# Optimization experiments

Hardware: AMD Instinct MI355X
Metric: run time of the kernel (lower is better)

Reference implementation:

```python
import jax, jax.numpy as jnp
import numpy as np

# Model / shape constants (match init_kwargs and input_specs)
E, H, N, B = 1024, 16, 4096, 4
D = E // H               # head_dim = 64
W_SZ, EXT, C_SZ = 128, 128, 128   # window, ext window, rf chunk
NEG = -1e9


def _linear(x, w, b):
    # torch nn.Linear convention: w is (out, in)
    return x @ w.T + b


def _layernorm(x, g, b, eps=1e-5):
    m = jnp.mean(x, -1, keepdims=True)
    v = jnp.mean((x - m) ** 2, -1, keepdims=True)
    return (x - m) * jax.lax.rsqrt(v + eps) * g + b


def _ext_windows(x, w, ext):
    # x: (b,h,n,d) -> (b,h,g,ext+w,d); window g covers keys [g*w-ext, g*w+w)
    # (front-padded with zeros, same as causal_window_1d_partition + as_strided)
    g = x.shape[2] // w
    xp = jnp.pad(x, ((0, 0), (0, 0), (ext, 0), (0, 0)))
    idx = jnp.arange(g)[:, None] * w + jnp.arange(ext + w)[None, :]
    return xp[:, :, idx]


def setup_inputs() -> dict:
    key = jax.random.key(0)
    ks = jax.random.split(key, 20)
    p = lambda i, shape: jax.random.normal(ks[i], shape, jnp.float32) * 0.02
    return {
        'query': jax.random.normal(ks[0], (N, B, E), jnp.float32),
        'Wq': p(1, (E, E)), 'bq': jnp.zeros((E,), jnp.float32),
        'Wk': p(2, (E, E)), 'bk': jnp.zeros((E,), jnp.float32),
        'Wv': p(3, (E, E)), 'bv': jnp.zeros((E,), jnp.float32),
        'Wo': p(4, (E, E)), 'bo': jnp.zeros((E,), jnp.float32),
        'mu_q_w': p(5, (D, D)), 'mu_q_b': jnp.zeros((D,), jnp.float32),
        'mu_q_g': jnp.ones((D,), jnp.float32), 'mu_q_be': jnp.zeros((D,), jnp.float32),
        'mu_k_w': p(6, (D, D)), 'mu_k_b': jnp.zeros((D,), jnp.float32),
        'mu_k_g': jnp.ones((D,), jnp.float32), 'mu_k_be': jnp.zeros((D,), jnp.float32),
    }


def reference(query, Wq, bq, Wk, bk, Wv, bv, Wo, bo,
              mu_q_w, mu_q_b, mu_q_g, mu_q_be,
              mu_k_w, mu_k_b, mu_k_g, mu_k_be):
    n, b, e = query.shape
    h, d = H, D
    scaling = d ** -0.5

    q = _linear(query, Wq, bq)
    k = _linear(query, Wk, bk)
    v = _linear(query, Wv, bv)
    to_bhnd = lambda t: jnp.transpose(t.reshape(n, b, h, d), (1, 2, 0, 3))
    q, k, v = to_bhnd(q), to_bhnd(k), to_bhnd(v)
    q = q * scaling

    # ---------------- local causal windowed attention scores ----------------
    g = n // W_SZ
    w_q = q.reshape(b, h, g, W_SZ, d)
    w_k = _ext_windows(k, W_SZ, EXT)   # (b,h,g,EXT+W,d)
    w_v = _ext_windows(v, W_SZ, EXT)
    local_dots = jnp.einsum('bhgid,bhgjd->bhgij', w_q, w_k)
    i = jnp.arange(W_SZ)[:, None]
    j = jnp.arange(EXT + W_SZ)[None, :]
    causal_ok = j <= i + EXT                      # key pos <= query pos
    gi = jnp.arange(g)[:, None, None]
    valid = j[None] >= (EXT - gi * W_SZ)          # mask zero-padded front keys
    local_mask = causal_ok[None] & valid          # (g, W, EXT+W)
    local_dots = jnp.where(local_mask[None, None], local_dots, NEG)

    # ------------- random-feature (EVA) chunk-level global branch -------------
    nc = n // C_SZ
    rf_q = q.reshape(b, h, nc, C_SZ, d)
    rf_k = k.reshape(b, h, nc, C_SZ, d)
    rf_v = v.reshape(b, h, nc, C_SZ, d)
    rf_q_bar = _layernorm(_linear(rf_q.mean(-2), mu_q_w, mu_q_b), mu_q_g, mu_q_be)
    rf_k_bar = _layernorm(_linear(rf_k.mean(-2), mu_k_w, mu_k_b), mu_k_g, mu_k_be)
    mu = rf_q_bar + rf_k_bar   # eval mode: weights = mu (no Gaussian noise)

    # prm_projection(rf_k, mu) with normalize=False, then softmax within chunk
    norm = scaling * jnp.sum(rf_k ** 2, -1) / 2.0            # (b,h,nc,p)
    log_proj_k = jnp.einsum('bhcd,bhcpd->bhcp', mu, rf_k) * scaling - norm
    beta = jax.nn.softmax(log_proj_k, -1)
    rfa_chunk = jnp.einsum('bhcp,bhcpd->bhcd', beta, rf_v)   # SNIS chunk values

    rfa_dots = jnp.einsum('bhgid,bhcd->bhgic', w_q, rf_k_bar)
    # chunk c visible to window g iff the whole chunk precedes the window
    chunk_vis = (jnp.arange(nc)[None, :] + 1) * C_SZ <= jnp.arange(g)[:, None] * W_SZ
    rfa_dots = jnp.where(chunk_vis[None, None, :, None, :], rfa_dots, NEG)

    # joint softmax over [local keys | global chunk pseudo-keys]
    attn = jax.nn.softmax(jnp.concatenate([local_dots, rfa_dots], -1), -1)
    la, ga = attn[..., : EXT + W_SZ], attn[..., EXT + W_SZ:]
    out = jnp.einsum('bhgij,bhgjd->bhgid', la, w_v) \
        + jnp.einsum('bhgic,bhcd->bhgid', ga, rfa_chunk)

    out = out.reshape(b, h, n, d)
    out = jnp.transpose(out, (2, 0, 1, 3)).reshape(n, b, e)
    return _linear(out, Wo, bo)
```

## Files before the change

kernel.cpp:

```cpp
#include <hip/hip_runtime.h>
#include <hip/hip_bf16.h>

typedef __hip_bfloat16 bf16;
typedef __attribute__((ext_vector_type(8))) short bf16x8;
typedef __attribute__((ext_vector_type(4))) float f32x4;

#define E_DIM 1024
#define H_DIM 16
#define N_DIM 4096
#define B_DIM 4
#define D_DIM 64
#define G_WIN 32
#define NC 32
#define M_ROWS 16384

#define AS1 __attribute__((address_space(1)))
#define AS3 __attribute__((address_space(3)))

__global__ __launch_bounds__(256) void cvt_f32_bf16(
    const float* __restrict__ in, bf16* __restrict__ out)
{
    int i = (blockIdx.x * 256 + threadIdx.x) * 8;
    float4 f0 = *(const float4*)(in + i);
    float4 f1 = *(const float4*)(in + i + 4);
    union { bf16 t[8]; uint4 u; } pk;
    pk.t[0] = (bf16)f0.x; pk.t[1] = (bf16)f0.y; pk.t[2] = (bf16)f0.z; pk.t[3] = (bf16)f0.w;
    pk.t[4] = (bf16)f1.x; pk.t[5] = (bf16)f1.y; pk.t[6] = (bf16)f1.z; pk.t[7] = (bf16)f1.w;
    *(uint4*)(out + i) = pk.u;
}

template<int MODE, bool WB16>
__global__ __launch_bounds__(256) void gemm_mfma(
    const bf16* __restrict__ A, const void* __restrict__ Wp,
    const float* __restrict__ bias, float scale,
    bf16* __restrict__ out_bf, float* __restrict__ out_f)
{
    __shared__ bf16 As[128 * 32];
    __shared__ bf16 Bs[128 * 32];
    int tid  = threadIdx.x;
    int lane = tid & 63;
    int wv   = tid >> 6;
    int wm   = (wv >> 1) * 64;
    int wn   = (wv & 1) * 64;
    int quad = lane >> 4;
    int l16  = lane & 15;

    int nwg = gridDim.x;
    int per = nwg >> 3;
    int logical = (blockIdx.x & 7) * per + (blockIdx.x >> 3);
    int col0 = (logical & 7) * 128;
    int row0 = (logical >> 3) * 128;

    f32x4 acc[4][4] = {};

    for (int k0 = 0; k0 < E_DIM; k0 += 32) {
#pragma unroll
        for (int i = 0; i < 2; i++) {
            int idx = tid + i * 256;
            int r = idx >> 2, c = idx & 3;
            const bf16* g = A + (size_t)(row0 + r) * E_DIM + k0 + c * 8;
            __builtin_amdgcn_global_load_lds(
                (const AS1 void*)g, (AS3 void*)(As + idx * 8), 16, 0, 0);
        }
        if constexpr (WB16) {
            const bf16* Wb = (const bf16*)Wp;
#pragma unroll
            for (int i = 0; i < 2; i++) {
                int idx = tid + i * 256;
                int e = idx >> 2, c = idx & 3;
                const bf16* g = Wb + (size_t)(col0 + e) * E_DIM + k0 + c * 8;
                __builtin_amdgcn_global_load_lds(
                    (const AS1 void*)g, (AS3 void*)(Bs + idx * 8), 16, 0, 0);
            }
        } else {
            const float* Wf = (const float*)Wp;
#pragma unroll
            for (int i = 0; i < 2; i++) {
                int idx = tid + i * 256;
                int e = idx >> 2, c = idx & 3;
                const float* wr = Wf + (size_t)(col0 + e) * E_DIM + k0 + c * 8;
                float4 f0 = *(const float4*)wr;
                float4 f1 = *(const float4*)(wr + 4);
                union { bf16 t[8]; uint4 u; } pk;
                pk.t[0] = (bf16)f0.x; pk.t[1] = (bf16)f0.y;
                pk.t[2] = (bf16)f0.z; pk.t[3] = (bf16)f0.w;
                pk.t[4] = (bf16)f1.x; pk.t[5] = (bf16)f1.y;
                pk.t[6] = (bf16)f1.z; pk.t[7] = (bf16)f1.w;
                *(uint4*)(Bs + idx * 8) = pk.u;
            }
        }
        __syncthreads();

        bf16x8 af[4], bfr[4];
#pragma unroll
        for (int t = 0; t < 4; t++) {
            af[t]  = *(const bf16x8*)(As + (wm + t * 16 + l16) * 32 + quad * 8);
            bfr[t] = *(const bf16x8*)(Bs + (wn + t * 16 + l16) * 32 + quad * 8);
        }
#pragma unroll
        for (int mt = 0; mt < 4; mt++)
#pragma unroll
            for (int nt = 0; nt < 4; nt++)
                acc[mt][nt] = __builtin_amdgcn_mfma_f32_16x16x32_bf16(
                    af[mt], bfr[nt], acc[mt][nt], 0, 0, 0);
        __syncthreads();
    }

#pragma unroll
    for (int mt = 0; mt < 4; mt++)
#pragma unroll
        for (int nt = 0; nt < 4; nt++)
#pragma unroll
            for (int rg = 0; rg < 4; rg++) {
                int m = row0 + wm + mt * 16 + quad * 4 + rg;
                int e = col0 + wn + nt * 16 + l16;
                float val = acc[mt][nt][rg];
                if (MODE == 0) {
                    float v2 = (val + bias[e]) * scale;
                    int n = m >> 2, bb = m & 3;
                    int h = e >> 6, d = e & 63;
                    out_bf[((((size_t)bb * H_DIM + h) * N_DIM + n) * D_DIM) + d] = (bf16)v2;
                } else {
                    out_f[(size_t)m * E_DIM + e] = val + bias[e];
                }
            }
}

__global__ __launch_bounds__(128) void chunk_stats(
    const bf16* __restrict__ q_s, const bf16* __restrict__ kbuf, const bf16* __restrict__ vbuf,
    const float* __restrict__ mqw, const float* __restrict__ mqb,
    const float* __restrict__ mqg, const float* __restrict__ mqbe,
    const float* __restrict__ mkw, const float* __restrict__ mkb,
    const float* __restrict__ mkg, const float* __restrict__ mkbe,
    float* __restrict__ rf_k_bar, float* __restrict__ rfa_chunk)
{
    int bid = blockIdx.x;
    int c = bid % NC;
    int bh = bid / NC;
    int tid = threadIdx.x;

    __shared__ float qm[64], km[64], qb_s[64], kb_s[64], mu_s[64], sc[128];
    __shared__ float stats[4];

    size_t base = ((size_t)bh * N_DIM + c * 128) * D_DIM;

    if (tid < 64) {
        float s = 0.f;
        for (int p = 0; p < 128; p++) s += (float)q_s[base + p * 64 + tid];
        qm[tid] = s * (1.0f / 128.0f);
    } else {
        int d = tid - 64;
        float s = 0.f;
        for (int p = 0; p < 128; p++) s += (float)kbuf[base + p * 64 + d];
        km[d] = s * (1.0f / 128.0f);
    }
    __syncthreads();

    if (tid < 64) {
        float t = mqb[tid];
        for (int d2 = 0; d2 < 64; d2++) t += qm[d2] * mqw[tid * 64 + d2];
        qb_s[tid] = t;
    } else {
        int d = tid - 64;
        float t = mkb[d];
        for (int d2 = 0; d2 < 64; d2++) t += km[d2] * mkw[d * 64 + d2];
        kb_s[d] = t;
    }
    __syncthreads();

    if (tid == 0) {
        float m = 0.f;
        for (int d = 0; d < 64; d++) m += qb_s[d];
        m *= (1.0f / 64.0f);
        float vv = 0.f;
        for (int d = 0; d < 64; d++) { float x = qb_s[d] - m; vv += x * x; }
        vv *= (1.0f / 64.0f);
        stats[0] = m; stats[1] = rsqrtf(vv + 1e-5f);
    } else if (tid == 64) {
        float m = 0.f;
        for (int d = 0; d < 64; d++) m += kb_s[d];
        m *= (1.0f / 64.0f);
        float vv = 0.f;
        for (int d = 0; d < 64; d++) { float x = kb_s[d] - m; vv += x * x; }
        vv *= (1.0f / 64.0f);
        stats[2] = m; stats[3] = rsqrtf(vv + 1e-5f);
    }
    __syncthreads();

    if (tid < 64) {
        float qn = (qb_s[tid] - stats[0]) * stats[1] * mqg[tid] + mqbe[tid];
        float kn = (kb_s[tid] - stats[2]) * stats[3] * mkg[tid] + mkbe[tid];
        mu_s[tid] = qn + kn;
        rf_k_bar[(size_t)bh * NC * 64 + c * 64 + tid] = kn;
    }
    __syncthreads();

    {
        float dot = 0.f, ss = 0.f;
        const bf16* kr = kbuf + base + tid * 64;
        for (int d = 0; d < 64; d++) {
            float kv = (float)kr[d];
            dot += mu_s[d] * kv;
            ss += kv * kv;
        }
        sc[tid] = dot * 0.125f - 0.125f * 0.5f * ss;
    }
    __syncthreads();
    if (tid == 0) {
        float m = sc[0];
        for (int p = 1; p < 128; p++) m = fmaxf(m, sc[p]);
        stats[0] = m;
    }
    __syncthreads();
    float e = expf(sc[tid] - stats[0]);
    sc[tid] = e;
    __syncthreads();
    if (tid == 0) {
        float s = 0.f;
        for (int p = 0; p < 128; p++) s += sc[p];
        stats[1] = 1.0f / s;
    }
    __syncthreads();
    sc[tid] *= stats[1];
    __syncthreads();

    if (tid < 64) {
        float acc = 0.f;
        for (int p = 0; p < 128; p++) acc += sc[p] * (float)vbuf[base + p * 64 + tid];
        rfa_chunk[(size_t)bh * NC * 64 + c * 64 + tid] = acc;
    }
}

__global__ __launch_bounds__(512, 4) void attn_kernel(
    const bf16* __restrict__ qin, const bf16* __restrict__ kbuf, const bf16* __restrict__ vbuf,
    const float* __restrict__ rf_k_bar, const float* __restrict__ rfa_chunk,
    bf16* __restrict__ aout)
{
    int bid = blockIdx.x;
    int g = bid & (G_WIN - 1);
    int bh = bid / G_WIN;
    int b = bh >> 4, h = bh & 15;
    int tid = threadIdx.x;
    int lane = tid & 63;
    int wv = tid >> 6;
    int q4 = lane >> 4;
    int l16 = lane & 15;

    __shared__ __align__(16) short Ks[288 * 72];
    __shared__ __align__(16) short Vt[64 * 296];

    size_t kvbase = (size_t)bh * N_DIM * D_DIM;
    int k0g = g * 128 - 128;

#pragma unroll
    for (int i = 0; i < 4; i++) {
        int ci = tid + i * 512;
        int key = ci >> 3, chc = ci & 7;
        int kidx = k0g + key; if (kidx < 0) kidx = 0;
        bf16x8 v = *(const bf16x8*)(kbuf + kvbase + (size_t)kidx * 64 + chc * 8);
        *(bf16x8*)(Ks + key * 72 + chc * 8) = v;
    }
    if (tid < 256) {
        int c = tid >> 3, chc = tid & 7;
        const float* src = rf_k_bar + (size_t)bh * NC * 64 + c * 64 + chc * 8;
        float4 f0 = *(const float4*)src;
        float4 f1 = *(const float4*)(src + 4);
        union { bf16 t[8]; bf16x8 v; } pk;
        pk.t[0] = (bf16)f0.x; pk.t[1] = (bf16)f0.y;
        pk.t[2] = (bf16)f0.z; pk.t[3] = (bf16)f0.w;
        pk.t[4] = (bf16)f1.x; pk.t[5] = (bf16)f1.y;
        pk.t[6] = (bf16)f1.z; pk.t[7] = (bf16)f1.w;
        *(bf16x8*)(Ks + (256 + c) * 72 + chc * 8) = pk.v;
    }
#pragma unroll
    for (int i = 0; i < 4; i++) {
        int ci = tid + i * 512;
        int key = ci & 255, dc = ci >> 8;
        int kidx = k0g + key; if (kidx < 0) kidx = 0;
        union { bf16x8 v; short s[8]; } u;
        u.v = *(const bf16x8*)(vbuf + kvbase + (size_t)kidx * 64 + dc * 8);
        int colp = (key & ~31) | (((key >> 2) & 3) << 3)
                 | (((key >> 4) & 1) << 2) | (key & 3);
#pragma unroll
        for (int jj = 0; jj < 8; jj++)
            Vt[(dc * 8 + jj) * 296 + colp] = u.s[jj];
    }
    if (tid < 256) {
        int d = tid >> 2, cg = tid & 3;
        const float* rc = rfa_chunk + (size_t)bh * NC * 64;
#pragma unroll
        for (int jj = 0; jj < 8; jj++) {
            int c = cg * 8 + jj;
            int p = (((c >> 2) & 3) << 3) | (((c >> 4) & 1) << 2) | (c & 3);
            union { bf16 bv; short s; } cv;
            cv.bv = (bf16)rc[(size_t)c * 64 + d];
            Vt[d * 296 + 256 + p] = cv.s;
        }
    }

    bf16x8 bq0, bq1;
    {
        const bf16* qrow = qin + kvbase + (size_t)(g * 128 + wv * 16 + l16) * 64 + q4 * 8;
        bq0 = *(const bf16x8*)qrow;
        bq1 = *(const bf16x8*)(qrow + 32);
    }

    __syncthreads();

    f32x4 acc[18] = {};
#pragma unroll
    for (int ct = 0; ct < 18; ct++) {
        int r = ct * 16 + l16;
        bf16x8 ak0 = *(const bf16x8*)(Ks + r * 72 + q4 * 8);
        bf16x8 ak1 = *(const bf16x8*)(Ks + r * 72 + 32 + q4 * 8);
        acc[ct] = __builtin_amdgcn_mfma_f32_16x16x32_bf16(ak0, bq0, acc[ct], 0, 0, 0);
        acc[ct] = __builtin_amdgcn_mfma_f32_16x16x32_bf16(ak1, bq1, acc[ct], 0, 0, 0);
    }

    int qi = wv * 16 + l16;
    float m = -1e30f;
#pragma unroll
    for (int ct = 0; ct < 18; ct++) {
        int jbase = ct * 16 + q4 * 4;
#pragma unroll
        for (int rg = 0; rg < 4; rg++) {
            int j = jbase + rg;
            bool ok = (j < 256) ? (k0g + j >= 0 && j <= qi + 128) : ((j - 256) < g);
            float s = ok ? acc[ct][rg] : -1e9f;
            acc[ct][rg] = s;
            m = fmaxf(m, s);
        }
    }
    m = fmaxf(m, __shfl_xor(m, 16));
    m = fmaxf(m, __shfl_xor(m, 32));

    float sum = 0.f;
#pragma unroll
    for (int ct = 0; ct < 18; ct++)
#pragma unroll
        for (int rg = 0; rg < 4; rg++) {
            float p = __expf(acc[ct][rg] - m);
            acc[ct][rg] = p;
            sum += p;
        }
    sum += __shfl_xor(sum, 16);
    sum += __shfl_xor(sum, 32);
    float rinv = 1.0f / sum;

    f32x4 accO[4] = {};
#pragma unroll
    for (int cc = 0; cc < 9; cc++) {
        union { bf16 t[8]; bf16x8 v; } pb;
#pragma unroll
        for (int e = 0; e < 4; e++) {
            pb.t[e]     = (bf16)acc[2 * cc][e];
            pb.t[4 + e] = (bf16)acc[2 * cc + 1][e];
        }
#pragma unroll
        for (int dt = 0; dt < 4; dt++) {
            bf16x8 av = *(const bf16x8*)(Vt + (dt * 16 + l16) * 296 + (cc * 4 + q4) * 8);
            accO[dt] = __builtin_amdgcn_mfma_f32_16x16x32_bf16(av, pb.v, accO[dt], 0, 0, 0);
        }
    }

    int nn = g * 128 + wv * 16 + l16;
    size_t obase = ((size_t)nn * B_DIM + b) * E_DIM + h * 64;
#pragma unroll
    for (int dt = 0; dt < 4; dt++) {
        union { bf16 t[4]; uint2 u; } o;
#pragma unroll
        for (int rg = 0; rg < 4; rg++) o.t[rg] = (bf16)(accO[dt][rg] * rinv);
        *(uint2*)(aout + obase + dt * 16 + q4 * 4) = o.u;
    }
}

extern "C" void kernel_launch(void* const* d_in, const int* in_sizes, int n_in,
                              void* d_out, int out_size, void* d_ws, size_t ws_size,
                              hipStream_t stream) {
    const float* query = (const float*)d_in[0];
    const float* Wq   = (const float*)d_in[1];
    const float* bq   = (const float*)d_in[2];
    const float* Wk   = (const float*)d_in[3];
    const float* bk   = (const float*)d_in[4];
    const float* Wv   = (const float*)d_in[5];
    const float* bv   = (const float*)d_in[6];
    const float* Wo   = (const float*)d_in[7];
    const float* bo   = (const float*)d_in[8];
    const float* mqw  = (const float*)d_in[9];
    const float* mqb  = (const float*)d_in[10];
    const float* mqg  = (const float*)d_in[11];
    const float* mqbe = (const float*)d_in[12];
    const float* mkw  = (const float*)d_in[13];
    const float* mkb  = (const float*)d_in[14];
    const float* mkg  = (const float*)d_in[15];
    const float* mkbe = (const float*)d_in[16];

    const size_t SZ = (size_t)B_DIM * H_DIM * N_DIM * D_DIM;
    const size_t STATS = (size_t)B_DIM * H_DIM * NC * D_DIM;

    bf16* kb = (bf16*)d_ws;
    bf16* vb = kb + SZ;
    float* rf_k_bar  = (float*)(vb + SZ);
    float* rfa_chunk = rf_k_bar + STATS;

    size_t base_bytes = 2 * SZ * sizeof(bf16) + 2 * STATS * sizeof(float);
    size_t wmat = (size_t)E_DIM * E_DIM;
    bool wb16   = ws_size >= base_bytes + 4 * wmat * sizeof(bf16);
    bool big_ws = ws_size >= base_bytes + 4 * wmat * sizeof(bf16) + SZ * sizeof(bf16);
    bf16* wq_b = (bf16*)((char*)d_ws + base_bytes);
    bf16* wk_b = wq_b + wmat;
    bf16* wv_b = wk_b + wmat;
    bf16* wo_b = wv_b + wmat;
    bf16* att_ws = wo_b + wmat;

    float* outf = (float*)d_out;
    bf16* qb  = (bf16*)d_out;
    bf16* qbf = qb + SZ;

    dim3 gblk(256);
    int ggrd = (E_DIM / 128) * (M_ROWS / 128);

    cvt_f32_bf16<<<(M_ROWS * E_DIM) / (256 * 8), 256, 0, stream>>>(query, qbf);
    if (wb16) {
        int wblk = (int)(wmat / (256 * 8));
        cvt_f32_bf16<<<wblk, 256, 0, stream>>>(Wq, wq_b);
        cvt_f32_bf16<<<wblk, 256, 0, stream>>>(Wk, wk_b);
        cvt_f32_bf16<<<wblk, 256, 0, stream>>>(Wv, wv_b);
        cvt_f32_bf16<<<wblk, 256, 0, stream>>>(Wo, wo_b);
    }

    if (wb16) {
        gemm_mfma<0, true><<<ggrd, gblk, 0, stream>>>(qbf, wq_b, bq, 0.125f, qb, nullptr);
        gemm_mfma<0, true><<<ggrd, gblk, 0, stream>>>(qbf, wk_b, bk, 1.0f, kb, nullptr);
        gemm_mfma<0, true><<<ggrd, gblk, 0, stream>>>(qbf, wv_b, bv, 1.0f, vb, nullptr);
    } else {
        gemm_mfma<0, false><<<ggrd, gblk, 0, stream>>>(qbf, Wq, bq, 0.125f, qb, nullptr);
        gemm_mfma<0, false><<<ggrd, gblk, 0, stream>>>(qbf, Wk, bk, 1.0f, kb, nullptr);
        gemm_mfma<0, false><<<ggrd, gblk, 0, stream>>>(qbf, Wv, bv, 1.0f, vb, nullptr);
    }

    chunk_stats<<<B_DIM * H_DIM * NC, 128, 0, stream>>>(
        qb, kb, vb, mqw, mqb, mqg, mqbe, mkw, mkb, mkg, mkbe, rf_k_bar, rfa_chunk);

    bf16* attn_dst = big_ws ? att_ws : qbf;
    attn_kernel<<<B_DIM * H_DIM * G_WIN, 512, 0, stream>>>(
        qb, kb, vb, rf_k_bar, rfa_chunk, attn_dst);

    const bf16* gemm_in;
    if (big_ws) {
        gemm_in = att_ws;
    } else {
        (void)hipMemcpyAsync(kb, qbf, SZ * sizeof(bf16), hipMemcpyDeviceToDevice, stream);
        gemm_in = kb;
    }

    if (wb16) {
        gemm_mfma<1, true><<<ggrd, gblk, 0, stream>>>(gemm_in, wo_b, bo, 1.0f, nullptr, outf);
    } else {
        gemm_mfma<1, false><<<ggrd, gblk, 0, stream>>>(gemm_in, Wo, bo, 1.0f, nullptr, outf);
    }
}
```

Before: 424.1 us.

## Fuse QKV projections into one GEMM, skip masked attention tiles, use wave reductions

The three Q/K/V projection GEMMs become a single launch with three times the grid. It reads the contiguous bf16 Wq/Wk/Wv buffers as one 3072-row weight and a concatenated bias copy, and routes each column tile to the q, k or v output with the right scale. The block-to-tile mapping is changed to an XCD-aware chunking. In the attention kernel, fully masked score and PV tiles are skipped using causal/visibility predicates, and s_setprio is raised around the MFMA loops. chunk_stats replaces serial single-thread layernorm and softmax reductions with wave shuffle reductions, adding three small bias memcpys per call.

After: 403.0 us. 5.0% less time.

```diff
diff --git a/kernel.cpp b/kernel.cpp
--- a/kernel.cpp
+++ b/kernel.cpp
@@ -33,7 +33,8 @@
 __global__ __launch_bounds__(256) void gemm_mfma(
     const bf16* __restrict__ A, const void* __restrict__ Wp,
     const float* __restrict__ bias, float scale,
-    bf16* __restrict__ out_bf, float* __restrict__ out_f)
+    bf16* __restrict__ out_bf, float* __restrict__ out_f,
+    bf16* __restrict__ out_k, bf16* __restrict__ out_v)
 {
     __shared__ bf16 As[128 * 32];
     __shared__ bf16 Bs[128 * 32];
@@ -45,11 +46,12 @@
     int quad = lane >> 4;
     int l16  = lane & 15;
 
-    int nwg = gridDim.x;
-    int per = nwg >> 3;
-    int logical = (blockIdx.x & 7) * per + (blockIdx.x >> 3);
-    int col0 = (logical & 7) * 128;
-    int row0 = (logical >> 3) * 128;
+    int chunk  = blockIdx.x & 7;
+    int lc     = blockIdx.x >> 3;
+    int colt   = lc >> 4;
+    int rowsub = lc & 15;
+    int col0 = colt * 128;
+    int row0 = (chunk * 16 + rowsub) * 128;
 
     f32x4 acc[4][4] = {};
 
@@ -106,6 +108,14 @@
         __syncthreads();
     }
 
+    bf16* dst = out_bf;
+    float scl = scale;
+    if (MODE == 2) {
+        int sel = col0 >> 10;
+        dst = (sel == 0) ? out_bf : ((sel == 1) ? out_k : out_v);
+        scl = (sel == 0) ? scale : 1.0f;
+    }
+
 #pragma unroll
     for (int mt = 0; mt < 4; mt++)
 #pragma unroll
@@ -115,13 +125,14 @@
                 int m = row0 + wm + mt * 16 + quad * 4 + rg;
                 int e = col0 + wn + nt * 16 + l16;
                 float val = acc[mt][nt][rg];
-                if (MODE == 0) {
-                    float v2 = (val + bias[e]) * scale;
+                if (MODE == 1) {
+                    out_f[(size_t)m * E_DIM + e] = val + bias[e];
+                } else {
+                    float v2 = (val + bias[e]) * scl;
+                    int el = e & 1023;
                     int n = m >> 2, bb = m & 3;
-                    int h = e >> 6, d = e & 63;
-                    out_bf[((((size_t)bb * H_DIM + h) * N_DIM + n) * D_DIM) + d] = (bf16)v2;
-                } else {
-                    out_f[(size_t)m * E_DIM + e] = val + bias[e];
+                    int h = el >> 6, d = el & 63;
+                    dst[((((size_t)bb * H_DIM + h) * N_DIM + n) * D_DIM) + d] = (bf16)v2;
                 }
             }
 }
@@ -138,9 +149,11 @@
     int c = bid % NC;
     int bh = bid / NC;
     int tid = threadIdx.x;
-
-    __shared__ float qm[64], km[64], qb_s[64], kb_s[64], mu_s[64], sc[128];
-    __shared__ float stats[4];
+    int lane = tid & 63;
+    int wid = tid >> 6;
+
+    __shared__ float qm[64], km[64], mu_s[64], sc[128];
+    __shared__ float parts[4];
 
     size_t base = ((size_t)bh * N_DIM + c * 128) * D_DIM;
 
@@ -156,45 +169,37 @@
     }
     __syncthreads();
 
-    if (tid < 64) {
-        float t = mqb[tid];
-        for (int d2 = 0; d2 < 64; d2++) t += qm[d2] * mqw[tid * 64 + d2];
-        qb_s[tid] = t;
-    } else {
-        int d = tid - 64;
-        float t = mkb[d];
-        for (int d2 = 0; d2 < 64; d2++) t += km[d2] * mkw[d * 64 + d2];
-        kb_s[d] = t;
+    {
+        float t;
+        if (wid == 0) {
+            t = mqb[lane];
+            for (int d2 = 0; d2 < 64; d2++) t += qm[d2] * mqw[lane * 64 + d2];
+        } else {
+            t = mkb[lane];
+            for (int d2 = 0; d2 < 64; d2++) t += km[d2] * mkw[lane * 64 + d2];
+        }
+        float s = t;
+        s += __shfl_xor(s, 1);  s += __shfl_xor(s, 2);  s += __shfl_xor(s, 4);
+        s += __shfl_xor(s, 8);  s += __shfl_xor(s, 16); s += __shfl_xor(s, 32);
+        float mean = s * (1.0f / 64.0f);
+        float x = t - mean;
+        float v2 = x * x;
+        v2 += __shfl_xor(v2, 1);  v2 += __shfl_xor(v2, 2);  v2 += __shfl_xor(v2, 4);
+        v2 += __shfl_xor(v2, 8);  v2 += __shfl_xor(v2, 16); v2 += __shfl_xor(v2, 32);
+        float rstd = rsqrtf(v2 * (1.0f / 64.0f) + 1e-5f);
+        if (wid == 0) {
+            qm[lane] = x * rstd * mqg[lane] + mqbe[lane];
+        } else {
+            float kn = x * rstd * mkg[lane] + mkbe[lane];
+            km[lane] = kn;
+            rf_k_bar[(size_t)bh * NC * 64 + c * 64 + lane] = kn;
+        }
     }
     __syncthreads();
-
-    if (tid == 0) {
-        float m = 0.f;
-        for (int d = 0; d < 64; d++) m += qb_s[d];
-        m *= (1.0f / 64.0f);
-        float vv = 0.f;
-        for (int d = 0; d < 64; d++) { float x = qb_s[d] - m; vv += x * x; }
-        vv *= (1.0f / 64.0f);
-        stats[0] = m; stats[1] = rsqrtf(vv + 1e-5f);
-    } else if (tid == 64) {
-        float m = 0.f;
-        for (int d = 0; d < 64; d++) m += kb_s[d];
-        m *= (1.0f / 64.0f);
-        float vv = 0.f;
-        for (int d = 0; d < 64; d++) { float x = kb_s[d] - m; vv += x * x; }
-        vv *= (1.0f / 64.0f);
-        stats[2] = m; stats[3] = rsqrtf(vv + 1e-5f);
-    }
+    if (tid < 64) mu_s[tid] = qm[tid] + km[tid];
     __syncthreads();
 
-    if (tid < 64) {
-        float qn = (qb_s[tid] - stats[0]) * stats[1] * mqg[tid] + mqbe[tid];
-        float kn = (kb_s[tid] - stats[2]) * stats[3] * mkg[tid] + mkbe[tid];
-        mu_s[tid] = qn + kn;
-        rf_k_bar[(size_t)bh * NC * 64 + c * 64 + tid] = kn;
-    }
-    __syncthreads();
-
+    float scv;
     {
         float dot = 0.f, ss = 0.f;
         const bf16* kr = kbuf + base + tid * 64;
@@ -203,25 +208,25 @@
             dot += mu_s[d] * kv;
             ss += kv * kv;
         }
-        sc[tid] = dot * 0.125f - 0.125f * 0.5f * ss;
-    }
-    __syncthreads();
-    if (tid == 0) {
-        float m = sc[0];
-        for (int p = 1; p < 128; p++) m = fmaxf(m, sc[p]);
-        stats[0] = m;
-    }
-    __syncthreads();
-    float e = expf(sc[tid] - stats[0]);
-    sc[tid] = e;
-    __syncthreads();
-    if (tid == 0) {
-        float s = 0.f;
-        for (int p = 0; p < 128; p++) s += sc[p];
-        stats[1] = 1.0f / s;
-    }
-    __syncthreads();
-    sc[tid] *= stats[1];
+        scv = dot * 0.125f - 0.0625f * ss;
+    }
+    {
+        float mv = scv;
+        mv = fmaxf(mv, __shfl_xor(mv, 1));  mv = fmaxf(mv, __shfl_xor(mv, 2));
+        mv = fmaxf(mv, __shfl_xor(mv, 4));  mv = fmaxf(mv, __shfl_xor(mv, 8));
+        mv = fmaxf(mv, __shfl_xor(mv, 16)); mv = fmaxf(mv, __shfl_xor(mv, 32));
+        if (lane == 0) parts[wid] = mv;
+        __syncthreads();
+        float mall = fmaxf(parts[0], parts[1]);
+        float e = expf(scv - mall);
+        float sv = e;
+        sv += __shfl_xor(sv, 1);  sv += __shfl_xor(sv, 2);  sv += __shfl_xor(sv, 4);
+        sv += __shfl_xor(sv, 8);  sv += __shfl_xor(sv, 16); sv += __shfl_xor(sv, 32);
+        if (lane == 0) parts[2 + wid] = sv;
+        __syncthreads();
+        float inv = 1.0f / (parts[2] + parts[3]);
+        sc[tid] = e * inv;
+    }
     __syncthreads();
 
     if (tid < 64) {
@@ -308,19 +313,27 @@
     __syncthreads();
 
     f32x4 acc[18] = {};
+    __builtin_amdgcn_s_setprio(1);
 #pragma unroll
     for (int ct = 0; ct < 18; ct++) {
+        bool live = (ct < 16) ? (ct <= wv + 8 && !(g == 0 && ct < 8))
+                              : ((ct == 16) ? (g > 0) : (g > 16));
+        if (!live) continue;
         int r = ct * 16 + l16;
         bf16x8 ak0 = *(const bf16x8*)(Ks + r * 72 + q4 * 8);
         bf16x8 ak1 = *(const bf16x8*)(Ks + r * 72 + 32 + q4 * 8);
         acc[ct] = __builtin_amdgcn_mfma_f32_16x16x32_bf16(ak0, bq0, acc[ct], 0, 0, 0);
         acc[ct] = __builtin_amdgcn_mfma_f32_16x16x32_bf16(ak1, bq1, acc[ct], 0, 0, 0);
     }
+    __builtin_amdgcn_s_setprio(0);
 
     int qi = wv * 16 + l16;
     float m = -1e30f;
 #pragma unroll
     for (int ct = 0; ct < 18; ct++) {
+        bool live = (ct < 16) ? (ct <= wv + 8 && !(g == 0 && ct < 8))
+                              : ((ct == 16) ? (g > 0) : (g > 16));
+        if (!live) continue;
         int jbase = ct * 16 + q4 * 4;
 #pragma unroll
         for (int rg = 0; rg < 4; rg++) {
@@ -336,20 +349,27 @@
 
     float sum = 0.f;
 #pragma unroll
-    for (int ct = 0; ct < 18; ct++)
+    for (int ct = 0; ct < 18; ct++) {
+        bool live = (ct < 16) ? (ct <= wv + 8 && !(g == 0 && ct < 8))
+                              : ((ct == 16) ? (g > 0) : (g > 16));
+        if (!live) continue;
 #pragma unroll
         for (int rg = 0; rg < 4; rg++) {
             float p = __expf(acc[ct][rg] - m);
             acc[ct][rg] = p;
             sum += p;
         }
+    }
     sum += __shfl_xor(sum, 16);
     sum += __shfl_xor(sum, 32);
     float rinv = 1.0f / sum;
 
     f32x4 accO[4] = {};
+    __builtin_amdgcn_s_setprio(1);
 #pragma unroll
     for (int cc = 0; cc < 9; cc++) {
+        bool live = (cc < 8) ? (2 * cc <= wv + 8 && !(g == 0 && cc < 4)) : (g > 0);
+        if (!live) continue;
         union { bf16 t[8]; bf16x8 v; } pb;
 #pragma unroll
         for (int e = 0; e < 4; e++) {
@@ -362,6 +382,7 @@
             accO[dt] = __builtin_amdgcn_mfma_f32_16x16x32_bf16(av, pb.v, accO[dt], 0, 0, 0);
         }
     }
+    __builtin_amdgcn_s_setprio(0);
 
     int nn = g * 128 + wv * 16 + l16;
     size_t obase = ((size_t)nn * B_DIM + b) * E_DIM + h * 64;
@@ -405,20 +426,23 @@
 
     size_t base_bytes = 2 * SZ * sizeof(bf16) + 2 * STATS * sizeof(float);
     size_t wmat = (size_t)E_DIM * E_DIM;
-    bool wb16   = ws_size >= base_bytes + 4 * wmat * sizeof(bf16);
-    bool big_ws = ws_size >= base_bytes + 4 * wmat * sizeof(bf16) + SZ * sizeof(bf16);
+    size_t wb16_bytes = base_bytes + 4 * wmat * sizeof(bf16) + 3072 * sizeof(float);
+    bool wb16   = ws_size >= wb16_bytes;
+    bool big_ws = ws_size >= wb16_bytes + SZ * sizeof(bf16);
     bf16* wq_b = (bf16*)((char*)d_ws + base_bytes);
     bf16* wk_b = wq_b + wmat;
     bf16* wv_b = wk_b + wmat;
     bf16* wo_b = wv_b + wmat;
-    bf16* att_ws = wo_b + wmat;
+    float* biasQKV = (float*)(wo_b + wmat);
+    bf16* att_ws = (bf16*)(biasQKV + 3072);
 
     float* outf = (float*)d_out;
     bf16* qb  = (bf16*)d_out;
     bf16* qbf = qb + SZ;
 
     dim3 gblk(256);
-    int ggrd = (E_DIM / 128) * (M_ROWS / 128);
+    int ggrd1 = (E_DIM / 128) * (M_ROWS / 128);
+    int ggrd3 = 3 * ggrd1;
 
     cvt_f32_bf16<<<(M_ROWS * E_DIM) / (256 * 8), 256, 0, stream>>>(query, qbf);
     if (wb16) {
@@ -427,16 +451,18 @@
         cvt_f32_bf16<<<wblk, 256, 0, stream>>>(Wk, wk_b);
         cvt_f32_bf16<<<wblk, 256, 0, stream>>>(Wv, wv_b);
         cvt_f32_bf16<<<wblk, 256, 0, stream>>>(Wo, wo_b);
+        (void)hipMemcpyAsync(biasQKV,        bq, 1024 * sizeof(float), hipMemcpyDeviceToDevice, stream);
+        (void)hipMemcpyAsync(biasQKV + 1024, bk, 1024 * sizeof(float), hipMemcpyDeviceToDevice, stream);
+        (void)hipMemcpyAsync(biasQKV + 2048, bv, 1024 * sizeof(float), hipMemcpyDeviceToDevice, stream);
     }
 
     if (wb16) {
-        gemm_mfma<0, true><<<ggrd, gblk, 0, stream>>>(qbf, wq_b, bq, 0.125f, qb, nullptr);
-        gemm_mfma<0, true><<<ggrd, gblk, 0, stream>>>(qbf, wk_b, bk, 1.0f, kb, nullptr);
-        gemm_mfma<0, true><<<ggrd, gblk, 0, stream>>>(qbf, wv_b, bv, 1.0f, vb, nullptr);
+        gemm_mfma<2, true><<<ggrd3, gblk, 0, stream>>>(
+            qbf, wq_b, biasQKV, 0.125f, qb, nullptr, kb, vb);
     } else {
-        gemm_mfma<0, false><<<ggrd, gblk, 0, stream>>>(qbf, Wq, bq, 0.125f, qb, nullptr);
-        gemm_mfma<0, false><<<ggrd, gblk, 0, stream>>>(qbf, Wk, bk, 1.0f, kb, nullptr);
-        gemm_mfma<0, false><<<ggrd, gblk, 0, stream>>>(qbf, Wv, bv, 1.0f, vb, nullptr);
+        gemm_mfma<0, false><<<ggrd1, gblk, 0, stream>>>(qbf, Wq, bq, 0.125f, qb, nullptr, nullptr, nullptr);
+        gemm_mfma<0, false><<<ggrd1, gblk, 0, stream>>>(qbf, Wk, bk, 1.0f, kb, nullptr, nullptr, nullptr);
+        gemm_mfma<0, false><<<ggrd1, gblk, 0, stream>>>(qbf, Wv, bv, 1.0f, vb, nullptr, nullptr, nullptr);
     }
 
     chunk_stats<<<B_DIM * H_DIM * NC, 128, 0, stream>>>(
@@ -455,8 +481,8 @@
     }
 
     if (wb16) {
-        gemm_mfma<1, true><<<ggrd, gblk, 0, stream>>>(gemm_in, wo_b, bo, 1.0f, nullptr, outf);
+        gemm_mfma<1, true><<<ggrd1, gblk, 0, stream>>>(gemm_in, wo_b, bo, 1.0f, nullptr, outf, nullptr, nullptr);
     } else {
-        gemm_mfma<1, false><<<ggrd, gblk, 0, stream>>>(gemm_in, Wo, bo, 1.0f, nullptr, outf);
+        gemm_mfma<1, false><<<ggrd1, gblk, 0, stream>>>(gemm_in, Wo, bo, 1.0f, nullptr, outf, nullptr, nullptr);
     }
 }
```
